# Kernel tuning notes

Measured on AMD Instinct MI355X. Metric: run time of the kernel, lower is better.

The kernel has to match this reference:

```python
import jax, jax.numpy as jnp
import numpy as np

DM = 128          # d_model (emb_dim)
VOCAB = 512       # len(id2word)
PAD = 0           # padding_idx
B = 64            # number of trees in the batch
# per-tree node counts by depth: 512 leaves, binary levels 256..1, unary root
COUNTS = [512, 256, 128, 64, 32, 16, 8, 4, 2, 1, 1]
_G = np.concatenate([[0], np.cumsum([B * c for c in COUNTS])]).astype(np.int64)
N = int(_G[-1])   # 65536 total nodes
NODES_PER_TREE = sum(COUNTS)  # 1024


def _build_indices():
    # level-major layout: global idx of node (level l, tree t, pos j) = _G[l] + t*COUNTS[l] + j
    left = np.zeros(N, np.int64)
    right = np.zeros(N, np.int64)
    for l in range(1, 11):
        c, cp = COUNTS[l], COUNTS[l - 1]
        t = np.repeat(np.arange(B), c)
        j = np.tile(np.arange(c), B)
        if l < 10:  # binary level: children are pairs in level l-1
            left[_G[l]:_G[l + 1]] = _G[l - 1] + t * cp + 2 * j
            right[_G[l]:_G[l + 1]] = _G[l - 1] + t * cp + 2 * j + 1
        else:       # unary root: single child is the level-9 node of the same tree
            left[_G[l]:_G[l + 1]] = _G[l - 1] + t * cp + j
    return left, right


def setup_inputs() -> dict:
    key = jax.random.key(0)
    ks = jax.random.split(key, 6)
    tokens = jax.random.randint(ks[0], (N,), 1, VOCAB)
    left_np, right_np = _build_indices()
    emb = jax.random.normal(ks[1], (VOCAB, DM), dtype=jnp.float32) * 0.5
    emb = emb.at[PAD].set(0.0)  # padding_idx row
    W_un = jax.random.normal(ks[2], (DM, 4 * DM), dtype=jnp.float32) / np.sqrt(DM)
    b_un = jax.random.normal(ks[3], (4 * DM,), dtype=jnp.float32) * 0.02
    W_bin = jax.random.normal(ks[4], (2 * DM, 5 * DM), dtype=jnp.float32) / np.sqrt(2 * DM)
    b_bin = jax.random.normal(ks[5], (5 * DM,), dtype=jnp.float32) * 0.02
    return {"tokens": tokens, "left_idx": jnp.asarray(left_np), "right_idx": jnp.asarray(right_np),
            "emb": emb, "W_un": W_un, "b_un": b_un, "W_bin": W_bin, "b_bin": b_bin}


def _embed(emb, idx):
    # Embedding lookup with max_norm=1.0 (rows renormalized to norm <= 1 on access)
    e = emb[idx]
    nrm = jnp.sqrt(jnp.sum(e * e, axis=-1, keepdims=True))
    return e * jnp.minimum(1.0, 1.0 / jnp.maximum(nrm, 1e-7))


def reference(tokens, left_idx, right_idx, emb, W_un, b_un, W_bin, b_bin):
    acts = jnp.zeros((N, 2, DM), dtype=emb.dtype)  # [node, (h,c), d]
    # depth 0: leaf embedding (op == -1); cell state stays zero
    acts = acts.at[0:int(_G[1]), 0].set(_embed(emb, tokens[0:int(_G[1])]))
    for l in range(1, 11):
        s, e = int(_G[l]), int(_G[l + 1])
        if l < 10:  # BinaryLSTM ('add')
            lch = acts[left_idx[s:e]]    # [n, 2, d] gather of child activations
            rch = acts[right_idx[s:e]]
            g = jnp.concatenate([lch[:, 0], rch[:, 0]], axis=-1) @ W_bin + b_bin
            i, o, u, fl, fr = jnp.split(g, 5, axis=-1)
            c = jax.nn.sigmoid(i) * jnp.tanh(u) \
                + jax.nn.sigmoid(fl) * lch[:, 1] + jax.nn.sigmoid(fr) * rch[:, 1]
        else:       # UnaryLSTM ('sin') at the root
            ch = acts[left_idx[s:e]]
            g = ch[:, 0] @ W_un + b_un
            i, o, u, f = jnp.split(g, 4, axis=-1)
            c = jax.nn.sigmoid(i) * jnp.tanh(u) + jax.nn.sigmoid(f) * ch[:, 1]
        h = jax.nn.sigmoid(o) * jnp.tanh(c)
        acts = acts.at[s:e].set(jnp.stack([h, c], axis=1))  # scatter back
    hidden = acts[:, 0, :]
    # split per tree and pad (equal lengths -> per-level reshape + concat), [B, 1024, d]
    parts = [hidden[int(_G[l]):int(_G[l + 1])].reshape(B, COUNTS[l], DM) for l in range(11)]
    return jnp.concatenate(parts, axis=1)
```

## Files before the change

### kernel.cpp

```cpp
#include <hip/hip_runtime.h>
#include <math.h>


typedef __attribute__((ext_vector_type(8))) short s8_t;
typedef __attribute__((ext_vector_type(4))) float f32x4;

#define PLANE_DELTA 8388608

__device__ __forceinline__ float sigf(float x){ return 1.0f/(1.0f+expf(-x)); }

__device__ __forceinline__ unsigned short f2bf_rne(float x){
    unsigned int u = __builtin_bit_cast(unsigned int, x);
    unsigned int r = (u + 0x7FFFu + ((u>>16)&1u)) >> 16;
    return (unsigned short)r;
}
__device__ __forceinline__ float bf2f(unsigned short b){
    return __builtin_bit_cast(float, ((unsigned int)b)<<16);
}
__device__ __forceinline__ void gl_lds16(const void* g, void* l){
    __builtin_amdgcn_global_load_lds(
        (const __attribute__((address_space(1))) unsigned int*)g,
        (__attribute__((address_space(3))) unsigned int*)l, 16, 0, 0);
}

__global__ __launch_bounds__(256) void prep_w(
    const float* __restrict__ W, unsigned short* __restrict__ Wext)
{
    int n = blockIdx.x;
    int k = threadIdx.x;
    float x = W[(size_t)k * 640 + n];
    unsigned short h = f2bf_rne(x);
    Wext[(size_t)n * 512 + k]       = h;
    Wext[(size_t)n * 512 + 256 + k] = f2bf_rne(x - bf2f(h));
}

__global__ __launch_bounds__(256) void leaf_kernel(
    const int* __restrict__ tokens, const float* __restrict__ emb,
    unsigned short* __restrict__ Hhi, float* __restrict__ C,
    float* __restrict__ out, int n_leaves)
{
    int node = blockIdx.x * 4 + (threadIdx.x >> 6);
    if (node >= n_leaves) return;
    int lane = threadIdx.x & 63;
    int tok = tokens[node];
    float2 e = *(const float2*)(emb + (size_t)tok * 128 + lane * 2);
    float ss = e.x * e.x + e.y * e.y;
#pragma unroll
    for (int off = 32; off; off >>= 1) ss += __shfl_xor(ss, off, 64);
    float nrm = sqrtf(ss);
    float scale = fminf(1.0f, 1.0f / fmaxf(nrm, 1e-7f));
    float hx = e.x * scale, hy = e.y * scale;
    unsigned short hxh = f2bf_rne(hx), hyh = f2bf_rne(hy);
    unsigned short hxl = f2bf_rne(hx - bf2f(hxh)), hyl = f2bf_rne(hy - bf2f(hyh));
    size_t p = (size_t)node * 128 + lane * 2;
    *(unsigned int*)(Hhi + p)               = (unsigned int)hxh | ((unsigned int)hyh << 16);
    *(unsigned int*)(Hhi + p + PLANE_DELTA) = (unsigned int)hxl | ((unsigned int)hyl << 16);
    *(float2*)(C + p) = make_float2(0.f, 0.f);
    int t = node >> 9, j = node & 511;
    *(float2*)(out + ((size_t)t * 1024 + j) * 128 + lane * 2) = make_float2(hx, hy);
}

__global__ __launch_bounds__(256, 2) void bin3(
    unsigned short* __restrict__ Hhi,
    float* __restrict__ C,
    const int* __restrict__ left, const int* __restrict__ right,
    const unsigned short* __restrict__ Wext, const float* __restrict__ bb,
    float* __restrict__ out,
    int s, int n_nodes, int out_off, int log2c)
{
    __shared__ __align__(16) unsigned short SL[4 * 9216];
    __shared__ __align__(16) unsigned short dmy[1024];
    __shared__ int sLR[256];

    const int tid  = threadIdx.x;
    const int lane = tid & 63;
    const int w    = tid >> 6;
    const int bm0  = blockIdx.x * 128;
    const int d0   = blockIdx.y * 32;

    if (tid < 128) {
        int r = bm0 + tid; if (r >= n_nodes) r = n_nodes - 1;
        sLR[tid]       = left[s + r];
        sLR[128 + tid] = right[s + r];
    }
    __syncthreads();

    int aOffL[2], aOffR[2];
#pragma unroll
    for (int j = 0; j < 2; ++j) {
        int ch = tid + j * 256, row = ch >> 2, slot = ch & 3;
        int g = slot ^ ((row >> 1) & 3);
        aOffL[j] = sLR[row] * 256 + g * 16;
        aOffR[j] = sLR[128 + row] * 256 + g * 16;
    }
    int bOff0, bOff1, bOff2;
    {
        int nn = tid >> 2, slot = tid & 3;
        int g = slot ^ ((nn >> 1) & 3);
        bOff0 = ((nn >> 5) * 128 + d0 + (nn & 31)) * 1024 + g * 16;
    }
    {
        int ch = tid + 256, nn = ch >> 2, slot = ch & 3;
        int g = slot ^ ((nn >> 1) & 3);
        bOff1 = ((nn >> 5) * 128 + d0 + (nn & 31)) * 1024 + g * 16;
    }
    if (tid < 128) {
        int ch = tid + 512, nn = ch >> 2, slot = ch & 3;
        int g = slot ^ ((nn >> 1) & 3);
        bOff2 = ((nn >> 5) * 128 + d0 + (nn & 31)) * 1024 + g * 16;
    } else {
        bOff2 = 0;
    }

    const char* HhiB  = (const char*)Hhi;
    const char* WextB = (const char*)Wext;

    f32x4 acc[2][10];
#pragma unroll
    for (int i = 0; i < 2; ++i)
#pragma unroll
        for (int j = 0; j < 10; ++j) acc[i][j] = f32x4{0.f, 0.f, 0.f, 0.f};

    auto stage = [&](int st, int buf) {
        const int tm    = st >> 3;
        const int k256  = (st & 7) * 32;
        const int side  = k256 >> 7;
        const int aoffB = ((tm == 2) ? PLANE_DELTA * 2 : 0) + (k256 & 127) * 2;
        const int koffB = ((tm == 1) ? (256 + k256) : k256) * 2;
        char* Abase = (char*)SL + buf * 18432;
        char* Bbase = Abase + 8192;
        const int a0 = side ? aOffR[0] : aOffL[0];
        const int a1 = side ? aOffR[1] : aOffL[1];
        gl_lds16(HhiB + (size_t)(a0 + aoffB), Abase + w * 1024);
        gl_lds16(HhiB + (size_t)(a1 + aoffB), Abase + 4096 + w * 1024);
        gl_lds16(WextB + (size_t)(bOff0 + koffB), Bbase + w * 1024);
        gl_lds16(WextB + (size_t)(bOff1 + koffB), Bbase + 4096 + w * 1024);
        gl_lds16(WextB + (size_t)(bOff2 + koffB),
                 (w < 2) ? (void*)(Bbase + 8192 + w * 1024)
                         : (void*)((char*)dmy + (w - 2) * 1024));
    };

    const int r15  = lane & 15;
    const int sl_  = (lane >> 4) ^ ((r15 >> 1) & 3);
    const int offA = w * 2048 + r15 * 64 + sl_ * 16;
    const int offB = r15 * 64 + sl_ * 16;

    stage(0, 0);
    stage(1, 1);
    stage(2, 2);
    int cbuf = 0, sbuf = 3;
#pragma unroll 1
    for (int st = 0; st < 24; ++st) {
        if (st <= 21)      asm volatile("s_waitcnt vmcnt(10)" ::: "memory");
        else if (st == 22) asm volatile("s_waitcnt vmcnt(5)"  ::: "memory");
        else               asm volatile("s_waitcnt vmcnt(0)"  ::: "memory");
        __builtin_amdgcn_sched_barrier(0);
        __builtin_amdgcn_s_barrier();
        __builtin_amdgcn_sched_barrier(0);
        if (st + 3 < 24) stage(st + 3, sbuf);
        const char* Ap = (const char*)SL + cbuf * 18432;
        const char* Bp = Ap + 8192;
        s8_t a0v = *(const s8_t*)(Ap + offA);
        s8_t a1v = *(const s8_t*)(Ap + offA + 1024);
#pragma unroll
        for (int fn = 0; fn < 10; ++fn) {
            s8_t bf = *(const s8_t*)(Bp + offB + fn * 1024);
            acc[0][fn] = __builtin_amdgcn_mfma_f32_16x16x32_bf16(a0v, bf, acc[0][fn], 0, 0, 0);
            acc[1][fn] = __builtin_amdgcn_mfma_f32_16x16x32_bf16(a1v, bf, acc[1][fn], 0, 0, 0);
        }
        cbuf = (cbuf == 3) ? 0 : cbuf + 1;
        sbuf = (sbuf == 3) ? 0 : sbuf + 1;
    }

    float bias[5][2];
#pragma unroll
    for (int g = 0; g < 5; ++g) {
        bias[g][0] = bb[g * 128 + d0 + r15];
        bias[g][1] = bb[g * 128 + d0 + 16 + r15];
    }
#pragma unroll
    for (int fm = 0; fm < 2; ++fm) {
        const int rb = w * 32 + fm * 16 + ((lane >> 4) << 2);
#pragma unroll
        for (int reg = 0; reg < 4; ++reg) {
            const int rl = rb + reg;
            const int nl = bm0 + rl;
            const bool valid = nl < n_nodes;
            const int node = s + (valid ? nl : 0);
            const int ln = sLR[rl], rn = sLR[128 + rl];
#pragma unroll
            for (int hi = 0; hi < 2; ++hi) {
                const int d = d0 + hi * 16 + r15;
                float gi  = acc[fm][0 + hi][reg] + bias[0][hi];
                float go  = acc[fm][2 + hi][reg] + bias[1][hi];
                float gu  = acc[fm][4 + hi][reg] + bias[2][hi];
                float gfl = acc[fm][6 + hi][reg] + bias[3][hi];
                float gfr = acc[fm][8 + hi][reg] + bias[4][hi];
                float lc = C[(size_t)ln * 128 + d];
                float rc = C[(size_t)rn * 128 + d];
                float c = sigf(gi) * tanhf(gu) + sigf(gfl) * lc + sigf(gfr) * rc;
                float h = sigf(go) * tanhf(c);
                if (valid) {
                    size_t p = (size_t)node * 128 + d;
                    unsigned short hh = f2bf_rne(h);
                    Hhi[p]               = hh;
                    Hhi[p + PLANE_DELTA] = f2bf_rne(h - bf2f(hh));
                    C[p] = c;
                    const int tt = nl >> log2c, j = nl & ((1 << log2c) - 1);
                    out[((size_t)tt * 1024 + out_off + j) * 128 + d] = h;
                }
            }
        }
    }
}

__global__ __launch_bounds__(256) void un_kernel(
    const unsigned short* __restrict__ Hhi, const float* __restrict__ C,
    const int* __restrict__ left,
    const float* __restrict__ Wu, const float* __restrict__ bu,
    float* __restrict__ out, int s, int out_off)
{
    __shared__ float sh[16 * 512];
    float* X = sh;
    const int tid = threadIdx.x;
    const int bm0 = blockIdx.x * 16;

    for (int i = tid; i < 16 * 128; i += 256) {
        int m = i >> 7, d = i & 127;
        int ch = left[s + bm0 + m];
        size_t p = (size_t)ch * 128 + d;
        X[m * 128 + d] = bf2f(Hhi[p]) + bf2f(Hhi[p + PLANE_DELTA]);
    }
    __syncthreads();

    float acc0[16], acc1[16];
#pragma unroll
    for (int m = 0; m < 16; ++m) { acc0[m] = 0.f; acc1[m] = 0.f; }

    for (int k4 = 0; k4 < 32; ++k4) {
        const int k = k4 * 4;
        float w0[4], w1[4];
#pragma unroll
        for (int r = 0; r < 4; ++r) {
            w0[r] = Wu[(k + r) * 512 + tid];
            w1[r] = Wu[(k + r) * 512 + tid + 256];
        }
#pragma unroll
        for (int m = 0; m < 16; ++m) {
            float4 xv = *(const float4*)(X + m * 128 + k);
            acc0[m] = fmaf(xv.x, w0[0], fmaf(xv.y, w0[1], fmaf(xv.z, w0[2], fmaf(xv.w, w0[3], acc0[m]))));
            acc1[m] = fmaf(xv.x, w1[0], fmaf(xv.y, w1[1], fmaf(xv.z, w1[2], fmaf(xv.w, w1[3], acc1[m]))));
        }
    }

    float b0 = bu[tid], b1 = bu[tid + 256];
    __syncthreads();
    float* Gm = sh;
#pragma unroll
    for (int m = 0; m < 16; ++m) {
        Gm[m * 512 + tid]       = acc0[m] + b0;
        Gm[m * 512 + tid + 256] = acc1[m] + b1;
    }
    __syncthreads();

    for (int i = tid; i < 16 * 128; i += 256) {
        int m = i >> 7, d = i & 127;
        const float* g = Gm + m * 512;
        float gi = g[d], go = g[128 + d], gu = g[256 + d], gf = g[384 + d];
        float cc = C[(size_t)left[s + bm0 + m] * 128 + d];
        float c = sigf(gi) * tanhf(gu) + sigf(gf) * cc;
        float h = sigf(go) * tanhf(c);
        out[((size_t)(bm0 + m) * 1024 + out_off) * 128 + d] = h;
    }
}

extern "C" void kernel_launch(void* const* d_in, const int* in_sizes, int n_in,
                              void* d_out, int out_size, void* d_ws, size_t ws_size,
                              hipStream_t stream) {
    const int*   tokens = (const int*)d_in[0];
    const int*   left   = (const int*)d_in[1];
    const int*   right  = (const int*)d_in[2];
    const float* emb    = (const float*)d_in[3];
    const float* W_un   = (const float*)d_in[4];
    const float* b_un   = (const float*)d_in[5];
    const float* W_bin  = (const float*)d_in[6];
    const float* b_bin  = (const float*)d_in[7];
    float* out = (float*)d_out;

    unsigned short* Hhi  = (unsigned short*)d_ws;
    float*          C    = (float*)((char*)d_ws + 33554432);
    unsigned short* Wext = (unsigned short*)((char*)d_ws + 67108864);

    static const int counts[11] = {512, 256, 128, 64, 32, 16, 8, 4, 2, 1, 1};
    static const int log2c[11]  = {9, 8, 7, 6, 5, 4, 3, 2, 1, 0, 0};
    int G[12]; G[0] = 0;
    for (int l = 0; l < 11; ++l) G[l + 1] = G[l] + 64 * counts[l];
    int off[11]; off[0] = 0;
    for (int l = 1; l < 11; ++l) off[l] = off[l - 1] + counts[l - 1];

    prep_w<<<640, 256, 0, stream>>>(W_bin, Wext);
    leaf_kernel<<<G[1] / 4, 256, 0, stream>>>(tokens, emb, Hhi, C, out, G[1]);

    for (int l = 1; l < 10; ++l) {
        int n = 64 * counts[l];
        int gm = (n + 127) / 128;
        bin3<<<dim3(gm, 4), 256, 0, stream>>>(Hhi, C, left, right, Wext, b_bin,
                                              out, G[l], n, off[l], log2c[l]);
    }

    un_kernel<<<4, 256, 0, stream>>>(Hhi, C, left, W_un, b_un, out, G[10], off[10]);
}
```

Baseline: 350.8 us.

## Fuse all tree levels into one persistent kernel with grid barriers

Replaces the twelve separate launches (weight prep, leaf embedding, nine binary levels, unary root) with a single persistent kernel of 512 blocks that moves between levels through atomic-counter grid barriers. The goal is to remove per-launch overhead and idle gaps between the small, dependent level kernels. In exchange, every level now pays a grid-wide spin barrier. Correctness relies on all 512 blocks being co-resident, which __launch_bounds__(256,2) is meant to allow. Idle blocks still wait at each barrier, and the Wext prep now shares the first phase with the leaf work.

```diff
diff --git a/kernel.cpp b/kernel.cpp
--- a/kernel.cpp
+++ b/kernel.cpp
@@ -6,6 +6,7 @@
 typedef __attribute__((ext_vector_type(4))) float f32x4;
 
 #define PLANE_DELTA 8388608
+#define NB 512
 
 __device__ __forceinline__ float sigf(float x){ return 1.0f/(1.0f+expf(-x)); }
 
@@ -23,254 +24,272 @@
         (__attribute__((address_space(3))) unsigned int*)l, 16, 0, 0);
 }
 
-__global__ __launch_bounds__(256) void prep_w(
-    const float* __restrict__ W, unsigned short* __restrict__ Wext)
-{
-    int n = blockIdx.x;
-    int k = threadIdx.x;
-    float x = W[(size_t)k * 640 + n];
-    unsigned short h = f2bf_rne(x);
-    Wext[(size_t)n * 512 + k]       = h;
-    Wext[(size_t)n * 512 + 256 + k] = f2bf_rne(x - bf2f(h));
-}
-
-__global__ __launch_bounds__(256) void leaf_kernel(
-    const int* __restrict__ tokens, const float* __restrict__ emb,
-    unsigned short* __restrict__ Hhi, float* __restrict__ C,
-    float* __restrict__ out, int n_leaves)
-{
-    int node = blockIdx.x * 4 + (threadIdx.x >> 6);
-    if (node >= n_leaves) return;
-    int lane = threadIdx.x & 63;
-    int tok = tokens[node];
-    float2 e = *(const float2*)(emb + (size_t)tok * 128 + lane * 2);
-    float ss = e.x * e.x + e.y * e.y;
-#pragma unroll
-    for (int off = 32; off; off >>= 1) ss += __shfl_xor(ss, off, 64);
-    float nrm = sqrtf(ss);
-    float scale = fminf(1.0f, 1.0f / fmaxf(nrm, 1e-7f));
-    float hx = e.x * scale, hy = e.y * scale;
-    unsigned short hxh = f2bf_rne(hx), hyh = f2bf_rne(hy);
-    unsigned short hxl = f2bf_rne(hx - bf2f(hxh)), hyl = f2bf_rne(hy - bf2f(hyh));
-    size_t p = (size_t)node * 128 + lane * 2;
-    *(unsigned int*)(Hhi + p)               = (unsigned int)hxh | ((unsigned int)hyh << 16);
-    *(unsigned int*)(Hhi + p + PLANE_DELTA) = (unsigned int)hxl | ((unsigned int)hyl << 16);
-    *(float2*)(C + p) = make_float2(0.f, 0.f);
-    int t = node >> 9, j = node & 511;
-    *(float2*)(out + ((size_t)t * 1024 + j) * 128 + lane * 2) = make_float2(hx, hy);
-}
-
-__global__ __launch_bounds__(256, 2) void bin3(
-    unsigned short* __restrict__ Hhi,
-    float* __restrict__ C,
-    const int* __restrict__ left, const int* __restrict__ right,
-    const unsigned short* __restrict__ Wext, const float* __restrict__ bb,
-    float* __restrict__ out,
-    int s, int n_nodes, int out_off, int log2c)
+__device__ __forceinline__ void gridbar(unsigned int* cnt) {
+    __syncthreads();
+    if (threadIdx.x == 0) {
+        __hip_atomic_fetch_add(cnt, 1u, __ATOMIC_RELEASE, __HIP_MEMORY_SCOPE_AGENT);
+        while (__hip_atomic_load(cnt, __ATOMIC_RELAXED, __HIP_MEMORY_SCOPE_AGENT) < (unsigned)NB)
+            __builtin_amdgcn_s_sleep(8);
+        __threadfence();
+    }
+    __syncthreads();
+}
+
+__global__ void init_bar(unsigned int* bar) {
+    if (threadIdx.x < 16) bar[threadIdx.x] = 0;
+}
+
+__global__ __launch_bounds__(256, 2) void fused(
+    const int* __restrict__ tokens, const int* __restrict__ left,
+    const int* __restrict__ right, const float* __restrict__ emb,
+    const float* __restrict__ Wu, const float* __restrict__ bu,
+    const float* __restrict__ Wb, const float* __restrict__ bb,
+    float* __restrict__ out, unsigned short* __restrict__ Hhi,
+    float* __restrict__ C, unsigned short* __restrict__ Wext,
+    unsigned int* __restrict__ bar)
 {
     __shared__ __align__(16) unsigned short SL[4 * 9216];
     __shared__ __align__(16) unsigned short dmy[1024];
     __shared__ int sLR[256];
 
-    const int tid  = threadIdx.x;
-    const int lane = tid & 63;
-    const int w    = tid >> 6;
-    const int bm0  = blockIdx.x * 128;
-    const int d0   = blockIdx.y * 32;
-
-    if (tid < 128) {
-        int r = bm0 + tid; if (r >= n_nodes) r = n_nodes - 1;
-        sLR[tid]       = left[s + r];
-        sLR[128 + tid] = right[s + r];
-    }
-    __syncthreads();
-
-    int aOffL[2], aOffR[2];
-#pragma unroll
-    for (int j = 0; j < 2; ++j) {
-        int ch = tid + j * 256, row = ch >> 2, slot = ch & 3;
-        int g = slot ^ ((row >> 1) & 3);
-        aOffL[j] = sLR[row] * 256 + g * 16;
-        aOffR[j] = sLR[128 + row] * 256 + g * 16;
-    }
-    int bOff0, bOff1, bOff2;
-    {
-        int nn = tid >> 2, slot = tid & 3;
-        int g = slot ^ ((nn >> 1) & 3);
-        bOff0 = ((nn >> 5) * 128 + d0 + (nn & 31)) * 1024 + g * 16;
-    }
-    {
-        int ch = tid + 256, nn = ch >> 2, slot = ch & 3;
-        int g = slot ^ ((nn >> 1) & 3);
-        bOff1 = ((nn >> 5) * 128 + d0 + (nn & 31)) * 1024 + g * 16;
-    }
-    if (tid < 128) {
-        int ch = tid + 512, nn = ch >> 2, slot = ch & 3;
-        int g = slot ^ ((nn >> 1) & 3);
-        bOff2 = ((nn >> 5) * 128 + d0 + (nn & 31)) * 1024 + g * 16;
-    } else {
-        bOff2 = 0;
-    }
-
+    const int b = blockIdx.x, tid = threadIdx.x;
+    const int lane = tid & 63, w = tid >> 6;
     const char* HhiB  = (const char*)Hhi;
     const char* WextB = (const char*)Wext;
 
-    f32x4 acc[2][10];
-#pragma unroll
-    for (int i = 0; i < 2; ++i)
-#pragma unroll
-        for (int j = 0; j < 10; ++j) acc[i][j] = f32x4{0.f, 0.f, 0.f, 0.f};
-
-    auto stage = [&](int st, int buf) {
-        const int tm    = st >> 3;
-        const int k256  = (st & 7) * 32;
-        const int side  = k256 >> 7;
-        const int aoffB = ((tm == 2) ? PLANE_DELTA * 2 : 0) + (k256 & 127) * 2;
-        const int koffB = ((tm == 1) ? (256 + k256) : k256) * 2;
-        char* Abase = (char*)SL + buf * 18432;
-        char* Bbase = Abase + 8192;
-        const int a0 = side ? aOffR[0] : aOffL[0];
-        const int a1 = side ? aOffR[1] : aOffL[1];
-        gl_lds16(HhiB + (size_t)(a0 + aoffB), Abase + w * 1024);
-        gl_lds16(HhiB + (size_t)(a1 + aoffB), Abase + 4096 + w * 1024);
-        gl_lds16(WextB + (size_t)(bOff0 + koffB), Bbase + w * 1024);
-        gl_lds16(WextB + (size_t)(bOff1 + koffB), Bbase + 4096 + w * 1024);
-        gl_lds16(WextB + (size_t)(bOff2 + koffB),
-                 (w < 2) ? (void*)(Bbase + 8192 + w * 1024)
-                         : (void*)((char*)dmy + (w - 2) * 1024));
-    };
-
-    const int r15  = lane & 15;
-    const int sl_  = (lane >> 4) ^ ((r15 >> 1) & 3);
-    const int offA = w * 2048 + r15 * 64 + sl_ * 16;
-    const int offB = r15 * 64 + sl_ * 16;
-
-    stage(0, 0);
-    stage(1, 1);
-    stage(2, 2);
-    int cbuf = 0, sbuf = 3;
+    for (int idx = b * 256 + tid; idx < 640 * 256; idx += NB * 256) {
+        int nn = idx >> 8, k = idx & 255;
+        float x = Wb[k * 640 + nn];
+        unsigned short h = f2bf_rne(x);
+        Wext[nn * 512 + k]       = h;
+        Wext[nn * 512 + 256 + k] = f2bf_rne(x - bf2f(h));
+    }
+
+    {
+        int nbase = b * 64 + w * 16;
+        for (int i = 0; i < 16; ++i) {
+            int node = nbase + i;
+            int tok = tokens[node];
+            float2 e = *(const float2*)(emb + (size_t)tok * 128 + lane * 2);
+            float ss = e.x * e.x + e.y * e.y;
+#pragma unroll
+            for (int off = 32; off; off >>= 1) ss += __shfl_xor(ss, off, 64);
+            float nrm = sqrtf(ss);
+            float scale = fminf(1.0f, 1.0f / fmaxf(nrm, 1e-7f));
+            float hx = e.x * scale, hy = e.y * scale;
+            unsigned short hxh = f2bf_rne(hx), hyh = f2bf_rne(hy);
+            unsigned short hxl = f2bf_rne(hx - bf2f(hxh)), hyl = f2bf_rne(hy - bf2f(hyh));
+            size_t p = (size_t)node * 128 + lane * 2;
+            *(unsigned int*)(Hhi + p)               = (unsigned int)hxh | ((unsigned int)hyh << 16);
+            *(unsigned int*)(Hhi + p + PLANE_DELTA) = (unsigned int)hxl | ((unsigned int)hyl << 16);
+            *(float2*)(C + p) = make_float2(0.f, 0.f);
+            int t = node >> 9, j = node & 511;
+            *(float2*)(out + ((size_t)t * 1024 + j) * 128 + lane * 2) = make_float2(hx, hy);
+        }
+    }
+    gridbar(&bar[0]);
+
 #pragma unroll 1
-    for (int st = 0; st < 24; ++st) {
-        if (st <= 21)      asm volatile("s_waitcnt vmcnt(10)" ::: "memory");
-        else if (st == 22) asm volatile("s_waitcnt vmcnt(5)"  ::: "memory");
-        else               asm volatile("s_waitcnt vmcnt(0)"  ::: "memory");
-        __builtin_amdgcn_sched_barrier(0);
-        __builtin_amdgcn_s_barrier();
-        __builtin_amdgcn_sched_barrier(0);
-        if (st + 3 < 24) stage(st + 3, sbuf);
-        const char* Ap = (const char*)SL + cbuf * 18432;
-        const char* Bp = Ap + 8192;
-        s8_t a0v = *(const s8_t*)(Ap + offA);
-        s8_t a1v = *(const s8_t*)(Ap + offA + 1024);
-#pragma unroll
-        for (int fn = 0; fn < 10; ++fn) {
-            s8_t bf = *(const s8_t*)(Bp + offB + fn * 1024);
-            acc[0][fn] = __builtin_amdgcn_mfma_f32_16x16x32_bf16(a0v, bf, acc[0][fn], 0, 0, 0);
-            acc[1][fn] = __builtin_amdgcn_mfma_f32_16x16x32_bf16(a1v, bf, acc[1][fn], 0, 0, 0);
-        }
-        cbuf = (cbuf == 3) ? 0 : cbuf + 1;
-        sbuf = (sbuf == 3) ? 0 : sbuf + 1;
-    }
-
-    float bias[5][2];
-#pragma unroll
-    for (int g = 0; g < 5; ++g) {
-        bias[g][0] = bb[g * 128 + d0 + r15];
-        bias[g][1] = bb[g * 128 + d0 + 16 + r15];
-    }
-#pragma unroll
-    for (int fm = 0; fm < 2; ++fm) {
-        const int rb = w * 32 + fm * 16 + ((lane >> 4) << 2);
-#pragma unroll
-        for (int reg = 0; reg < 4; ++reg) {
-            const int rl = rb + reg;
-            const int nl = bm0 + rl;
-            const bool valid = nl < n_nodes;
-            const int node = s + (valid ? nl : 0);
-            const int ln = sLR[rl], rn = sLR[128 + rl];
-#pragma unroll
-            for (int hi = 0; hi < 2; ++hi) {
-                const int d = d0 + hi * 16 + r15;
-                float gi  = acc[fm][0 + hi][reg] + bias[0][hi];
-                float go  = acc[fm][2 + hi][reg] + bias[1][hi];
-                float gu  = acc[fm][4 + hi][reg] + bias[2][hi];
-                float gfl = acc[fm][6 + hi][reg] + bias[3][hi];
-                float gfr = acc[fm][8 + hi][reg] + bias[4][hi];
-                float lc = C[(size_t)ln * 128 + d];
-                float rc = C[(size_t)rn * 128 + d];
-                float c = sigf(gi) * tanhf(gu) + sigf(gfl) * lc + sigf(gfr) * rc;
-                float h = sigf(go) * tanhf(c);
-                if (valid) {
-                    size_t p = (size_t)node * 128 + d;
-                    unsigned short hh = f2bf_rne(h);
-                    Hhi[p]               = hh;
-                    Hhi[p + PLANE_DELTA] = f2bf_rne(h - bf2f(hh));
-                    C[p] = c;
-                    const int tt = nl >> log2c, j = nl & ((1 << log2c) - 1);
-                    out[((size_t)tt * 1024 + out_off + j) * 128 + d] = h;
+    for (int l = 1; l <= 9; ++l) {
+        const int n_nodes = 32768 >> l;
+        const int s       = 65536 - (65536 >> l);
+        const int ooff    = 1024 - (1024 >> l);
+        const int lg      = 9 - l;
+        const int Tx      = (n_nodes + 127) >> 7;
+        const int active  = Tx * 4;
+
+        if (b < active) {
+            int t = b;
+            if (active >= 8) { int q = active >> 3; t = (b & 7) * q + (b >> 3); }
+            const int bm0 = (t >> 2) * 128;
+            const int d0  = (t & 3) * 32;
+
+            if (tid < 128) {
+                int r = bm0 + tid; if (r >= n_nodes) r = n_nodes - 1;
+                sLR[tid]       = left[s + r];
+                sLR[128 + tid] = right[s + r];
+            }
+            __syncthreads();
+
+            int aOffL[2], aOffR[2];
+#pragma unroll
+            for (int j = 0; j < 2; ++j) {
+                int ch = tid + j * 256, row = ch >> 2, slot = ch & 3;
+                int g = slot ^ ((row >> 1) & 3);
+                aOffL[j] = sLR[row] * 256 + g * 16;
+                aOffR[j] = sLR[128 + row] * 256 + g * 16;
+            }
+            int bOff0, bOff1, bOff2;
+            {
+                int nn = tid >> 2, slot = tid & 3;
+                int g = slot ^ ((nn >> 1) & 3);
+                bOff0 = ((nn >> 5) * 128 + d0 + (nn & 31)) * 1024 + g * 16;
+            }
+            {
+                int ch = tid + 256, nn = ch >> 2, slot = ch & 3;
+                int g = slot ^ ((nn >> 1) & 3);
+                bOff1 = ((nn >> 5) * 128 + d0 + (nn & 31)) * 1024 + g * 16;
+            }
+            if (tid < 128) {
+                int ch = tid + 512, nn = ch >> 2, slot = ch & 3;
+                int g = slot ^ ((nn >> 1) & 3);
+                bOff2 = ((nn >> 5) * 128 + d0 + (nn & 31)) * 1024 + g * 16;
+            } else {
+                bOff2 = 0;
+            }
+
+            f32x4 acc[2][10];
+#pragma unroll
+            for (int i = 0; i < 2; ++i)
+#pragma unroll
+                for (int j = 0; j < 10; ++j) acc[i][j] = f32x4{0.f, 0.f, 0.f, 0.f};
+
+            auto stage = [&](int st, int buf) {
+                const int tm    = st >> 3;
+                const int k256  = (st & 7) * 32;
+                const int side  = k256 >> 7;
+                const int aoffB = ((tm == 2) ? PLANE_DELTA * 2 : 0) + (k256 & 127) * 2;
+                const int koffB = ((tm == 1) ? (256 + k256) : k256) * 2;
+                char* Abase = (char*)SL + buf * 18432;
+                char* Bbase = Abase + 8192;
+                const int a0 = side ? aOffR[0] : aOffL[0];
+                const int a1 = side ? aOffR[1] : aOffL[1];
+                gl_lds16(HhiB + (size_t)(a0 + aoffB), Abase + w * 1024);
+                gl_lds16(HhiB + (size_t)(a1 + aoffB), Abase + 4096 + w * 1024);
+                gl_lds16(WextB + (size_t)(bOff0 + koffB), Bbase + w * 1024);
+                gl_lds16(WextB + (size_t)(bOff1 + koffB), Bbase + 4096 + w * 1024);
+                gl_lds16(WextB + (size_t)(bOff2 + koffB),
+                         (w < 2) ? (void*)(Bbase + 8192 + w * 1024)
+                                 : (void*)((char*)dmy + (w - 2) * 1024));
+            };
+
+            const int r15  = lane & 15;
+            const int sl_  = (lane >> 4) ^ ((r15 >> 1) & 3);
+            const int offA = w * 2048 + r15 * 64 + sl_ * 16;
+            const int offB = r15 * 64 + sl_ * 16;
+
+            stage(0, 0);
+            stage(1, 1);
+            stage(2, 2);
+            int cbuf = 0, sbuf = 3;
+#pragma unroll 1
+            for (int st = 0; st < 24; ++st) {
+                if (st <= 21)      asm volatile("s_waitcnt vmcnt(10)" ::: "memory");
+                else if (st == 22) asm volatile("s_waitcnt vmcnt(5)"  ::: "memory");
+                else               asm volatile("s_waitcnt vmcnt(0)"  ::: "memory");
+                __builtin_amdgcn_sched_barrier(0);
+                __builtin_amdgcn_s_barrier();
+                __builtin_amdgcn_sched_barrier(0);
+                if (st + 3 < 24) stage(st + 3, sbuf);
+                const char* Ap = (const char*)SL + cbuf * 18432;
+                const char* Bp = Ap + 8192;
+                s8_t a0v = *(const s8_t*)(Ap + offA);
+                s8_t a1v = *(const s8_t*)(Ap + offA + 1024);
+#pragma unroll
+                for (int fn = 0; fn < 10; ++fn) {
+                    s8_t bf = *(const s8_t*)(Bp + offB + fn * 1024);
+                    acc[0][fn] = __builtin_amdgcn_mfma_f32_16x16x32_bf16(a0v, bf, acc[0][fn], 0, 0, 0);
+                    acc[1][fn] = __builtin_amdgcn_mfma_f32_16x16x32_bf16(a1v, bf, acc[1][fn], 0, 0, 0);
                 }
-            }
-        }
-    }
-}
-
-__global__ __launch_bounds__(256) void un_kernel(
-    const unsigned short* __restrict__ Hhi, const float* __restrict__ C,
-    const int* __restrict__ left,
-    const float* __restrict__ Wu, const float* __restrict__ bu,
-    float* __restrict__ out, int s, int out_off)
-{
-    __shared__ float sh[16 * 512];
-    float* X = sh;
-    const int tid = threadIdx.x;
-    const int bm0 = blockIdx.x * 16;
-
-    for (int i = tid; i < 16 * 128; i += 256) {
-        int m = i >> 7, d = i & 127;
-        int ch = left[s + bm0 + m];
-        size_t p = (size_t)ch * 128 + d;
-        X[m * 128 + d] = bf2f(Hhi[p]) + bf2f(Hhi[p + PLANE_DELTA]);
-    }
-    __syncthreads();
-
-    float acc0[16], acc1[16];
-#pragma unroll
-    for (int m = 0; m < 16; ++m) { acc0[m] = 0.f; acc1[m] = 0.f; }
-
-    for (int k4 = 0; k4 < 32; ++k4) {
-        const int k = k4 * 4;
-        float w0[4], w1[4];
-#pragma unroll
-        for (int r = 0; r < 4; ++r) {
-            w0[r] = Wu[(k + r) * 512 + tid];
-            w1[r] = Wu[(k + r) * 512 + tid + 256];
-        }
+                cbuf = (cbuf == 3) ? 0 : cbuf + 1;
+                sbuf = (sbuf == 3) ? 0 : sbuf + 1;
+            }
+
+            float bias[5][2];
+#pragma unroll
+            for (int g = 0; g < 5; ++g) {
+                bias[g][0] = bb[g * 128 + d0 + r15];
+                bias[g][1] = bb[g * 128 + d0 + 16 + r15];
+            }
+#pragma unroll
+            for (int fm = 0; fm < 2; ++fm) {
+                const int rb = w * 32 + fm * 16 + ((lane >> 4) << 2);
+#pragma unroll
+                for (int reg = 0; reg < 4; ++reg) {
+                    const int rl = rb + reg;
+                    const int nl = bm0 + rl;
+                    const bool valid = nl < n_nodes;
+                    const int node = s + (valid ? nl : 0);
+                    const int ln = sLR[rl], rn = sLR[128 + rl];
+#pragma unroll
+                    for (int hi = 0; hi < 2; ++hi) {
+                        const int d = d0 + hi * 16 + r15;
+                        float gi  = acc[fm][0 + hi][reg] + bias[0][hi];
+                        float go  = acc[fm][2 + hi][reg] + bias[1][hi];
+                        float gu  = acc[fm][4 + hi][reg] + bias[2][hi];
+                        float gfl = acc[fm][6 + hi][reg] + bias[3][hi];
+                        float gfr = acc[fm][8 + hi][reg] + bias[4][hi];
+                        float lc = C[(size_t)ln * 128 + d];
+                        float rc = C[(size_t)rn * 128 + d];
+                        float c = sigf(gi) * tanhf(gu) + sigf(gfl) * lc + sigf(gfr) * rc;
+                        float h = sigf(go) * tanhf(c);
+                        if (valid) {
+                            size_t p = (size_t)node * 128 + d;
+                            unsigned short hh = f2bf_rne(h);
+                            Hhi[p]               = hh;
+                            Hhi[p + PLANE_DELTA] = f2bf_rne(h - bf2f(hh));
+                            C[p] = c;
+                            const int tt = nl >> lg, j = nl & ((1 << lg) - 1);
+                            out[((size_t)tt * 1024 + ooff + j) * 128 + d] = h;
+                        }
+                    }
+                }
+            }
+        }
+        gridbar(&bar[l]);
+    }
+
+    if (b < 4) {
+        float* X = (float*)SL;
+        const int bm0 = b * 16;
+        const int s10 = 65472;
+        for (int i = tid; i < 16 * 128; i += 256) {
+            int m = i >> 7, d = i & 127;
+            int ch = left[s10 + bm0 + m];
+            size_t p = (size_t)ch * 128 + d;
+            X[m * 128 + d] = bf2f(Hhi[p]) + bf2f(Hhi[p + PLANE_DELTA]);
+        }
+        __syncthreads();
+
+        float acc0[16], acc1[16];
+#pragma unroll
+        for (int m = 0; m < 16; ++m) { acc0[m] = 0.f; acc1[m] = 0.f; }
+
+        for (int k4 = 0; k4 < 32; ++k4) {
+            const int k = k4 * 4;
+            float w0[4], w1[4];
+#pragma unroll
+            for (int r = 0; r < 4; ++r) {
+                w0[r] = Wu[(k + r) * 512 + tid];
+                w1[r] = Wu[(k + r) * 512 + tid + 256];
+            }
+#pragma unroll
+            for (int m = 0; m < 16; ++m) {
+                float4 xv = *(const float4*)(X + m * 128 + k);
+                acc0[m] = fmaf(xv.x, w0[0], fmaf(xv.y, w0[1], fmaf(xv.z, w0[2], fmaf(xv.w, w0[3], acc0[m]))));
+                acc1[m] = fmaf(xv.x, w1[0], fmaf(xv.y, w1[1], fmaf(xv.z, w1[2], fmaf(xv.w, w1[3], acc1[m]))));
+            }
+        }
+
+        float b0 = bu[tid], b1 = bu[tid + 256];
+        __syncthreads();
+        float* Gm = (float*)SL;
 #pragma unroll
         for (int m = 0; m < 16; ++m) {
-            float4 xv = *(const float4*)(X + m * 128 + k);
-            acc0[m] = fmaf(xv.x, w0[0], fmaf(xv.y, w0[1], fmaf(xv.z, w0[2], fmaf(xv.w, w0[3], acc0[m]))));
-            acc1[m] = fmaf(xv.x, w1[0], fmaf(xv.y, w1[1], fmaf(xv.z, w1[2], fmaf(xv.w, w1[3], acc1[m]))));
-        }
-    }
-
-    float b0 = bu[tid], b1 = bu[tid + 256];
-    __syncthreads();
-    float* Gm = sh;
-#pragma unroll
-    for (int m = 0; m < 16; ++m) {
-        Gm[m * 512 + tid]       = acc0[m] + b0;
-        Gm[m * 512 + tid + 256] = acc1[m] + b1;
-    }
-    __syncthreads();
-
-    for (int i = tid; i < 16 * 128; i += 256) {
-        int m = i >> 7, d = i & 127;
-        const float* g = Gm + m * 512;
-        float gi = g[d], go = g[128 + d], gu = g[256 + d], gf = g[384 + d];
-        float cc = C[(size_t)left[s + bm0 + m] * 128 + d];
-        float c = sigf(gi) * tanhf(gu) + sigf(gf) * cc;
-        float h = sigf(go) * tanhf(c);
-        out[((size_t)(bm0 + m) * 1024 + out_off) * 128 + d] = h;
+            Gm[m * 512 + tid]       = acc0[m] + b0;
+            Gm[m * 512 + tid + 256] = acc1[m] + b1;
+        }
+        __syncthreads();
+
+        for (int i = tid; i < 16 * 128; i += 256) {
+            int m = i >> 7, d = i & 127;
+            const float* g = Gm + m * 512;
+            float gi = g[d], go = g[128 + d], gu = g[256 + d], gf = g[384 + d];
+            float cc = C[(size_t)left[s10 + bm0 + m] * 128 + d];
+            float c = sigf(gi) * tanhf(gu) + sigf(gf) * cc;
+            float h = sigf(go) * tanhf(c);
+            out[((size_t)(bm0 + m) * 1024 + 1023) * 128 + d] = h;
+        }
     }
 }
 
@@ -290,23 +309,9 @@
     unsigned short* Hhi  = (unsigned short*)d_ws;
     float*          C    = (float*)((char*)d_ws + 33554432);
     unsigned short* Wext = (unsigned short*)((char*)d_ws + 67108864);
-
-    static const int counts[11] = {512, 256, 128, 64, 32, 16, 8, 4, 2, 1, 1};
-    static const int log2c[11]  = {9, 8, 7, 6, 5, 4, 3, 2, 1, 0, 0};
-    int G[12]; G[0] = 0;
-    for (int l = 0; l < 11; ++l) G[l + 1] = G[l] + 64 * counts[l];
-    int off[11]; off[0] = 0;
-    for (int l = 1; l < 11; ++l) off[l] = off[l - 1] + counts[l - 1];
-
-    prep_w<<<640, 256, 0, stream>>>(W_bin, Wext);
-    leaf_kernel<<<G[1] / 4, 256, 0, stream>>>(tokens, emb, Hhi, C, out, G[1]);
-
-    for (int l = 1; l < 10; ++l) {
-        int n = 64 * counts[l];
-        int gm = (n + 127) / 128;
-        bin3<<<dim3(gm, 4), 256, 0, stream>>>(Hhi, C, left, right, Wext, b_bin,
-                                              out, G[l], n, off[l], log2c[l]);
-    }
-
-    un_kernel<<<4, 256, 0, stream>>>(Hhi, C, left, W_un, b_un, out, G[10], off[10]);
-}
+    unsigned int*   bar  = (unsigned int*)((char*)d_ws + 71303168);
+
+    init_bar<<<1, 64, 0, stream>>>(bar);
+    fused<<<NB, 256, 0, stream>>>(tokens, left, right, emb, W_un, b_un,
+                                  W_bin, b_bin, out, Hhi, C, Wext, bar);
+}
```

New measurement: 682.9 us. +94.7%, slower.
